# Performance work log

Measured on AMD Instinct MI355X. Metric: run time of the kernel, lower is better.

The kernel has to match this reference:

```python
import jax, jax.numpy as jnp
import numpy as np

# Dropout layers are treated as identity (eval mode) for a deterministic reference.

def _branch(x, Ws):
    # pattern in original: relu -> (dropout) -> linear, repeated; last linear has no trailing relu
    for W in Ws:
        x = jax.nn.relu(x) @ W.T
    return x

def _cross_mul(s, e):
    # z[k,h] = sum_j s[k,h]*e[k,j] = s[k,h] * sum_j e[k,j]
    return s * jnp.sum(e, axis=-1, keepdims=True)

def setup_inputs() -> dict:
    key = jax.random.key(0)
    ks = jax.random.split(key, 12)
    def lin(k, out_d, in_d):
        return jax.random.normal(k, (out_d, in_d), dtype=jnp.float32) * (1.0 / np.sqrt(in_d))
    B = 65536
    return {
        "result": jax.random.normal(ks[0], (B, 4, 768), dtype=jnp.float32),
        "sW1": lin(ks[1], 96, 768), "sW2": lin(ks[2], 48, 96), "sW3": lin(ks[3], 24, 48),
        "sW4": lin(ks[4], 12, 24), "sW5": lin(ks[5], 2, 12),
        "eW1": lin(ks[6], 96, 768), "eW2": lin(ks[7], 48, 96), "eW3": lin(ks[8], 24, 48),
        "eW4": lin(ks[9], 12, 24), "eW5": lin(ks[10], 8, 12),
        "s_seq": jnp.array([0.25, 0.25, 0.25, 0.25], dtype=jnp.float32),
        "s_pair": jnp.array([0.5, 0.5], dtype=jnp.float32),
        "e_seq": jnp.array([0.25, 0.25, 0.25, 0.25], dtype=jnp.float32),
        "e_pair": jnp.array([0.5, 0.5], dtype=jnp.float32),
        "cross_w": jnp.array([0.5, 0.5], dtype=jnp.float32),
    }

def reference(result, sW1, sW2, sW3, sW4, sW5, eW1, eW2, eW3, eW4, eW5,
              s_seq, s_pair, e_seq, e_pair, cross_w):
    sWs = (sW1, sW2, sW3, sW4, sW5)
    eWs = (eW1, eW2, eW3, eW4, eW5)
    # soft attention pools over the 4 "token" slots
    pair_e = result[:, 0, :] * e_pair[0] + result[:, 2, :] * e_pair[1]
    pair_s = result[:, 0, :] * s_pair[0] + result[:, 2, :] * s_pair[1]
    seq_e = jnp.einsum('bsd,s->bd', result, e_seq)
    seq_s = jnp.einsum('bsd,s->bd', result, s_seq)
    pair_e_out = _branch(pair_e, eWs)  # [B, 8]
    pair_s_out = _branch(pair_s, sWs)  # [B, 2]
    seq_e_out = _branch(seq_e, eWs)    # [B, 8]
    seq_s_out = _branch(seq_s, sWs)    # [B, 2]
    pair_cross = _cross_mul(pair_s_out, pair_e_out)
    seq_cross = _cross_mul(seq_s_out, seq_e_out)
    return cross_w[0] * pair_cross + cross_w[1] * seq_cross
```

## Files before the change

kernel.cpp:

```cpp
#include <hip/hip_runtime.h>

typedef _Float16 half8 __attribute__((ext_vector_type(8)));
typedef float floatx4 __attribute__((ext_vector_type(4)));

#define MFMA16(a, b, c) __builtin_amdgcn_mfma_f32_16x16x32_f16((a), (b), (c), 0, 0, 0)

#define OFF_W1 0
#define OFF_W2 147456
#define OFF_W3 156672
#define OFF_W4 160768
#define OFF_W5 161792

typedef __attribute__((address_space(3))) unsigned int lds_uint;
typedef __attribute__((address_space(1))) unsigned int glob_uint;

__device__ __forceinline__ void async_copy16(const void* g, void* l) {
    __builtin_amdgcn_global_load_lds((const glob_uint*)g, (lds_uint*)l, 16, 0, 0);
}

__global__ __launch_bounds__(64) void prep_weights(
    const float* __restrict__ eW1, const float* __restrict__ sW1,
    const float* __restrict__ eW2, const float* __restrict__ sW2,
    const float* __restrict__ eW3, const float* __restrict__ sW3,
    const float* __restrict__ eW4, const float* __restrict__ sW4,
    const float* __restrict__ eW5, const float* __restrict__ sW5,
    _Float16* __restrict__ ws)
{
    int b = blockIdx.x;
    int lane = threadIdx.x;
    const float* src;
    _Float16* dst;
    int N, K, nt, ks;
    if (b < 288) {
        int mat = b / 144, r = b % 144;
        nt = r / 24; ks = r % 24;
        src = mat ? sW1 : eW1; N = 96; K = 768;
        dst = ws + OFF_W1 + (size_t)((mat * 6 + nt) * 24 + ks) * 512;
    } else if (b < 306) {
        int i = b - 288, mat = i / 9, r = i % 9;
        nt = r / 3; ks = r % 3;
        src = mat ? sW2 : eW2; N = 48; K = 96;
        dst = ws + OFF_W2 + (size_t)((mat * 3 + nt) * 3 + ks) * 512;
    } else if (b < 314) {
        int i = b - 306, mat = i / 4, r = i % 4;
        nt = r / 2; ks = r % 2;
        src = mat ? sW3 : eW3; N = 24; K = 48;
        dst = ws + OFF_W3 + (size_t)((mat * 2 + nt) * 2 + ks) * 512;
    } else if (b < 316) {
        int mat = b - 314;
        nt = 0; ks = 0;
        src = mat ? sW4 : eW4; N = 12; K = 24;
        dst = ws + OFF_W4 + (size_t)mat * 512;
    } else {
        int mat = b - 316;
        nt = 0; ks = 0;
        src = mat ? sW5 : eW5; N = mat ? 2 : 8; K = 12;
        dst = ws + OFF_W5 + (size_t)mat * 512;
    }
    int n = nt * 16 + (lane & 15);
    int kb = ks * 32 + (lane >> 4) * 8;
    for (int j = 0; j < 8; ++j) {
        int k = kb + j;
        float v = (n < N && k < K) ? src[n * K + k] : 0.0f;
        dst[lane * 8 + j] = (_Float16)v;
    }
}

__device__ __forceinline__ const float4* rawp(const unsigned char* buf, int s, int t, int k16) {
    return (const float4*)(buf + ((s >> 1) * 1040 + ((s & 1) << 9) + (((t << 3) | k16) << 4)));
}

__device__ __forceinline__ half8 frag_pair(const unsigned char* buf, int s, int q,
                                           float w0, float w1) {
    float4 a0 = *rawp(buf, s, 0, 2 * q);
    float4 a1 = *rawp(buf, s, 0, 2 * q + 1);
    float4 c0 = *rawp(buf, s, 2, 2 * q);
    float4 c1 = *rawp(buf, s, 2, 2 * q + 1);
    half8 h;
    h[0] = (_Float16)fmaxf(w0 * a0.x + w1 * c0.x, 0.f);
    h[1] = (_Float16)fmaxf(w0 * a0.y + w1 * c0.y, 0.f);
    h[2] = (_Float16)fmaxf(w0 * a0.z + w1 * c0.z, 0.f);
    h[3] = (_Float16)fmaxf(w0 * a0.w + w1 * c0.w, 0.f);
    h[4] = (_Float16)fmaxf(w0 * a1.x + w1 * c1.x, 0.f);
    h[5] = (_Float16)fmaxf(w0 * a1.y + w1 * c1.y, 0.f);
    h[6] = (_Float16)fmaxf(w0 * a1.z + w1 * c1.z, 0.f);
    h[7] = (_Float16)fmaxf(w0 * a1.w + w1 * c1.w, 0.f);
    return h;
}

__device__ __forceinline__ half8 frag_seq(const unsigned char* buf, int s, int q,
                                          float w0, float w1, float w2, float w3) {
    float4 a0 = *rawp(buf, s, 0, 2 * q);
    float4 a1 = *rawp(buf, s, 0, 2 * q + 1);
    float4 b0 = *rawp(buf, s, 1, 2 * q);
    float4 b1 = *rawp(buf, s, 1, 2 * q + 1);
    float4 c0 = *rawp(buf, s, 2, 2 * q);
    float4 c1 = *rawp(buf, s, 2, 2 * q + 1);
    float4 d0 = *rawp(buf, s, 3, 2 * q);
    float4 d1 = *rawp(buf, s, 3, 2 * q + 1);
    half8 h;
    h[0] = (_Float16)fmaxf(w0 * a0.x + w1 * b0.x + w2 * c0.x + w3 * d0.x, 0.f);
    h[1] = (_Float16)fmaxf(w0 * a0.y + w1 * b0.y + w2 * c0.y + w3 * d0.y, 0.f);
    h[2] = (_Float16)fmaxf(w0 * a0.z + w1 * b0.z + w2 * c0.z + w3 * d0.z, 0.f);
    h[3] = (_Float16)fmaxf(w0 * a0.w + w1 * b0.w + w2 * c0.w + w3 * d0.w, 0.f);
    h[4] = (_Float16)fmaxf(w0 * a1.x + w1 * b1.x + w2 * c1.x + w3 * d1.x, 0.f);
    h[5] = (_Float16)fmaxf(w0 * a1.y + w1 * b1.y + w2 * c1.y + w3 * d1.y, 0.f);
    h[6] = (_Float16)fmaxf(w0 * a1.z + w1 * b1.z + w2 * c1.z + w3 * d1.z, 0.f);
    h[7] = (_Float16)fmaxf(w0 * a1.w + w1 * b1.w + w2 * c1.w + w3 * d1.w, 0.f);
    return h;
}

__global__ __launch_bounds__(256, 4) void fused_net(
    const float* __restrict__ result,
    const float* __restrict__ e_pair, const float* __restrict__ s_pair,
    const float* __restrict__ e_seq,  const float* __restrict__ s_seq,
    const float* __restrict__ cross_w,
    const _Float16* __restrict__ ws,
    float* __restrict__ out)
{
    __shared__ __align__(16) unsigned char lds_raw[35840];
    float* EoLDS = (float*)(lds_raw + 33280);
    float* SoLDS = (float*)(lds_raw + 33280 + 2048);

    const int tid  = threadIdx.x;
    const int lane = tid & 63;
    const int wave = tid >> 6;
    const int l15  = lane & 15;
    const int q    = lane >> 4;
    const int mat  = wave >> 1;
    const int mh   = wave & 1;
    const int sbase = blockIdx.x * 32;

    float w0, w1, w2 = 0.f, w3 = 0.f;
    if (mh == 0) {
        w0 = mat ? s_pair[0] : e_pair[0];
        w1 = mat ? s_pair[1] : e_pair[1];
    } else {
        w0 = mat ? s_seq[0] : e_seq[0];
        w1 = mat ? s_seq[1] : e_seq[1];
        w2 = mat ? s_seq[2] : e_seq[2];
        w3 = mat ? s_seq[3] : e_seq[3];
    }

    const floatx4 zf4 = {0.f, 0.f, 0.f, 0.f};

    const int dma_so  = lane >> 5;
    const int dma_u   = lane & 31;
    const int dma_t   = dma_u >> 3;
    const int dma_k16 = dma_u & 7;
    const size_t dma_goff = (size_t)(dma_t * 768 + dma_k16 * 4);

    floatx4 acc[2][6];
#pragma unroll
    for (int m = 0; m < 2; ++m)
#pragma unroll
        for (int n = 0; n < 6; ++n) acc[m][n] = zf4;

    const half8* Bw1 = (const half8*)(ws + OFF_W1) + (size_t)mat * (6 * 24 * 64);

    {
        const float* gbase = result + (size_t)sbase * 3072;
#pragma unroll
        for (int i = 0; i < 4; ++i) {
            int blk = wave * 4 + i;
            const float* g = gbase + (size_t)(2 * blk + dma_so) * 3072 + dma_goff;
            async_copy16(g, lds_raw + blk * 1040);
        }
    }
    __syncthreads();

#pragma unroll 2
    for (int c = 0; c < 24; ++c) {
        const unsigned char* cur = lds_raw + (c & 1) * 16640;
        unsigned char* nxt = lds_raw + ((c + 1) & 1) * 16640;
        if (c < 23) {
            const float* gbase = result + (size_t)sbase * 3072 + (c + 1) * 32;
#pragma unroll
            for (int i = 0; i < 4; ++i) {
                int blk = wave * 4 + i;
                const float* g = gbase + (size_t)(2 * blk + dma_so) * 3072 + dma_goff;
                async_copy16(g, nxt + blk * 1040);
            }
        }
        half8 a0f, a1f;
        if (mh == 0) {
            a0f = frag_pair(cur, l15,      q, w0, w1);
            a1f = frag_pair(cur, l15 + 16, q, w0, w1);
        } else {
            a0f = frag_seq(cur, l15,      q, w0, w1, w2, w3);
            a1f = frag_seq(cur, l15 + 16, q, w0, w1, w2, w3);
        }
#pragma unroll
        for (int nt = 0; nt < 6; ++nt) {
            half8 bf = Bw1[(nt * 24 + c) * 64 + lane];
            acc[0][nt] = MFMA16(a0f, bf, acc[0][nt]);
            acc[1][nt] = MFMA16(a1f, bf, acc[1][nt]);
        }
        __syncthreads();
    }

    _Float16* Y = (_Float16*)lds_raw;

#pragma unroll
    for (int m = 0; m < 2; ++m)
#pragma unroll
        for (int nt = 0; nt < 6; ++nt)
#pragma unroll
            for (int r = 0; r < 4; ++r) {
                int row = mat * 64 + mh * 32 + m * 16 + q * 4 + r;
                Y[row * 104 + nt * 16 + l15] = (_Float16)fmaxf(acc[m][nt][r], 0.f);
            }
    __syncthreads();

    floatx4 acc2[2][3];
#pragma unroll
    for (int m = 0; m < 2; ++m)
#pragma unroll
        for (int n = 0; n < 3; ++n) acc2[m][n] = zf4;
    {
        const _Float16* A2 = Y + mat * 64 * 104;
        const half8* Bw2 = (const half8*)(ws + OFF_W2) + (size_t)mat * (3 * 3 * 64);
#pragma unroll
        for (int ks2 = 0; ks2 < 3; ++ks2) {
            half8 a0 = *(const half8*)(A2 + (mh * 32 + l15) * 104 + ks2 * 32 + q * 8);
            half8 a1 = *(const half8*)(A2 + (mh * 32 + 16 + l15) * 104 + ks2 * 32 + q * 8);
#pragma unroll
            for (int nt = 0; nt < 3; ++nt) {
                half8 bf = Bw2[(nt * 3 + ks2) * 64 + lane];
                acc2[0][nt] = MFMA16(a0, bf, acc2[0][nt]);
                acc2[1][nt] = MFMA16(a1, bf, acc2[1][nt]);
            }
        }
    }
    __syncthreads();
#pragma unroll
    for (int m = 0; m < 2; ++m)
#pragma unroll
        for (int nt = 0; nt < 3; ++nt)
#pragma unroll
            for (int r = 0; r < 4; ++r) {
                int row = mat * 64 + mh * 32 + m * 16 + q * 4 + r;
                Y[row * 72 + nt * 16 + l15] = (_Float16)fmaxf(acc2[m][nt][r], 0.f);
            }
    for (int i = tid; i < 2048; i += 256) {
        int row = i >> 4;
        Y[row * 72 + 48 + (i & 15)] = (_Float16)0.f;
    }
    __syncthreads();

    floatx4 acc3[2][2];
#pragma unroll
    for (int m = 0; m < 2; ++m)
#pragma unroll
        for (int n = 0; n < 2; ++n) acc3[m][n] = zf4;
    {
        const _Float16* A3 = Y + mat * 64 * 72;
        const half8* Bw3 = (const half8*)(ws + OFF_W3) + (size_t)mat * (2 * 2 * 64);
#pragma unroll
        for (int ks2 = 0; ks2 < 2; ++ks2) {
            half8 a0 = *(const half8*)(A3 + (mh * 32 + l15) * 72 + ks2 * 32 + q * 8);
            half8 a1 = *(const half8*)(A3 + (mh * 32 + 16 + l15) * 72 + ks2 * 32 + q * 8);
#pragma unroll
            for (int nt = 0; nt < 2; ++nt) {
                half8 bf = Bw3[(nt * 2 + ks2) * 64 + lane];
                acc3[0][nt] = MFMA16(a0, bf, acc3[0][nt]);
                acc3[1][nt] = MFMA16(a1, bf, acc3[1][nt]);
            }
        }
    }
    __syncthreads();
#pragma unroll
    for (int m = 0; m < 2; ++m)
#pragma unroll
        for (int nt = 0; nt < 2; ++nt)
#pragma unroll
            for (int r = 0; r < 4; ++r) {
                int row = mat * 64 + mh * 32 + m * 16 + q * 4 + r;
                Y[row * 40 + nt * 16 + l15] = (_Float16)fmaxf(acc3[m][nt][r], 0.f);
            }
    for (int i = tid; i < 1024; i += 256) {
        int row = i >> 3;
        Y[row * 40 + 24 + (i & 7)] = (_Float16)0.f;
    }
    __syncthreads();

    floatx4 acc4[2];
    {
        const _Float16* A4 = Y + mat * 64 * 40;
        const half8* Bw4 = (const half8*)(ws + OFF_W4) + (size_t)mat * 64;
        half8 a0 = *(const half8*)(A4 + (mh * 32 + l15) * 40 + q * 8);
        half8 a1 = *(const half8*)(A4 + (mh * 32 + 16 + l15) * 40 + q * 8);
        half8 bf = Bw4[lane];
        acc4[0] = MFMA16(a0, bf, zf4);
        acc4[1] = MFMA16(a1, bf, zf4);
    }
    __syncthreads();
#pragma unroll
    for (int m = 0; m < 2; ++m)
#pragma unroll
        for (int r = 0; r < 4; ++r) {
            int row = mat * 64 + mh * 32 + m * 16 + q * 4 + r;
            Y[row * 40 + l15] = (_Float16)fmaxf(acc4[m][r], 0.f);
        }
    for (int i = tid; i < 2560; i += 256) {
        int row = i / 20;
        Y[row * 40 + 12 + (i % 20)] = (_Float16)0.f;
    }
    __syncthreads();

    floatx4 acc5[2];
    {
        const _Float16* A5 = Y + mat * 64 * 40;
        const half8* Bw5 = (const half8*)(ws + OFF_W5) + (size_t)mat * 64;
        half8 a0 = *(const half8*)(A5 + (mh * 32 + l15) * 40 + q * 8);
        half8 a1 = *(const half8*)(A5 + (mh * 32 + 16 + l15) * 40 + q * 8);
        half8 bf = Bw5[lane];
        acc5[0] = MFMA16(a0, bf, zf4);
        acc5[1] = MFMA16(a1, bf, zf4);
    }
    if (mat == 0) {
        if (l15 < 8) {
#pragma unroll
            for (int m = 0; m < 2; ++m)
#pragma unroll
                for (int r = 0; r < 4; ++r) {
                    int row = mh * 32 + m * 16 + q * 4 + r;
                    EoLDS[row * 8 + l15] = acc5[m][r];
                }
        }
    } else {
        if (l15 < 2) {
#pragma unroll
            for (int m = 0; m < 2; ++m)
#pragma unroll
                for (int r = 0; r < 4; ++r) {
                    int row = mh * 32 + m * 16 + q * 4 + r;
                    SoLDS[row * 2 + l15] = acc5[m][r];
                }
        }
    }
    __syncthreads();

    if (tid < 64) {
        int sample = tid >> 1;
        int h = tid & 1;
        float cw0 = cross_w[0], cw1 = cross_w[1];
        float pes = 0.f, ses = 0.f;
#pragma unroll
        for (int j = 0; j < 8; ++j) {
            pes += EoLDS[sample * 8 + j];
            ses += EoLDS[(32 + sample) * 8 + j];
        }
        float v = cw0 * SoLDS[sample * 2 + h] * pes
                + cw1 * SoLDS[(32 + sample) * 2 + h] * ses;
        out[(size_t)(sbase + sample) * 2 + h] = v;
    }
}

extern "C" void kernel_launch(void* const* d_in, const int* in_sizes, int n_in,
                              void* d_out, int out_size, void* d_ws, size_t ws_size,
                              hipStream_t stream) {
    (void)n_in; (void)out_size; (void)ws_size;
    const float* result = (const float*)d_in[0];
    const float* sW1 = (const float*)d_in[1];
    const float* sW2 = (const float*)d_in[2];
    const float* sW3 = (const float*)d_in[3];
    const float* sW4 = (const float*)d_in[4];
    const float* sW5 = (const float*)d_in[5];
    const float* eW1 = (const float*)d_in[6];
    const float* eW2 = (const float*)d_in[7];
    const float* eW3 = (const float*)d_in[8];
    const float* eW4 = (const float*)d_in[9];
    const float* eW5 = (const float*)d_in[10];
    const float* s_seq  = (const float*)d_in[11];
    const float* s_pair = (const float*)d_in[12];
    const float* e_seq  = (const float*)d_in[13];
    const float* e_pair = (const float*)d_in[14];
    const float* cross_w = (const float*)d_in[15];
    _Float16* ws = (_Float16*)d_ws;
    float* out = (float*)d_out;

    int B = in_sizes[0] / 3072;

    prep_weights<<<dim3(318), dim3(64), 0, stream>>>(
        eW1, sW1, eW2, sW2, eW3, sW3, eW4, sW4, eW5, sW5, ws);

    fused_net<<<dim3(B / 32), dim3(256), 0, stream>>>(
        result, e_pair, s_pair, e_seq, s_seq, cross_w, ws, out);
}
```

Before: 1.060 ms.

## Replace LDS double-buffered async staging with direct global loads and wave shuffles

The first-layer input staging no longer uses global_load_lds double buffering into LDS with per-chunk block barriers. Each wave now loads its rows straight from global memory into registers, computes the pooled ReLU values, packs them to fp16, and rearranges them into MFMA fragment layout with cross-lane shuffles. This removes the LDS traffic and the 24 __syncthreads in the K loop and shrinks LDS use. In exchange it loses explicit prefetch overlap, adds shuffle work, and all four waves now load the input independently (pair and seq waves reread the same data), raising global/L2 traffic. The occupancy hint drops from 4 to 3 blocks per SIMD.

```diff
diff --git a/kernel.cpp b/kernel.cpp
--- a/kernel.cpp
+++ b/kernel.cpp
@@ -10,13 +10,6 @@
 #define OFF_W3 156672
 #define OFF_W4 160768
 #define OFF_W5 161792
-
-typedef __attribute__((address_space(3))) unsigned int lds_uint;
-typedef __attribute__((address_space(1))) unsigned int glob_uint;
-
-__device__ __forceinline__ void async_copy16(const void* g, void* l) {
-    __builtin_amdgcn_global_load_lds((const glob_uint*)g, (lds_uint*)l, 16, 0, 0);
-}
 
 __global__ __launch_bounds__(64) void prep_weights(
     const float* __restrict__ eW1, const float* __restrict__ sW1,
@@ -66,51 +59,14 @@
     }
 }
 
-__device__ __forceinline__ const float4* rawp(const unsigned char* buf, int s, int t, int k16) {
-    return (const float4*)(buf + ((s >> 1) * 1040 + ((s & 1) << 9) + (((t << 3) | k16) << 4)));
+__device__ __forceinline__ unsigned int packh(float a, float b) {
+    union { _Float16 h[2]; unsigned int u; } x;
+    x.h[0] = (_Float16)a;
+    x.h[1] = (_Float16)b;
+    return x.u;
 }
 
-__device__ __forceinline__ half8 frag_pair(const unsigned char* buf, int s, int q,
-                                           float w0, float w1) {
-    float4 a0 = *rawp(buf, s, 0, 2 * q);
-    float4 a1 = *rawp(buf, s, 0, 2 * q + 1);
-    float4 c0 = *rawp(buf, s, 2, 2 * q);
-    float4 c1 = *rawp(buf, s, 2, 2 * q + 1);
-    half8 h;
-    h[0] = (_Float16)fmaxf(w0 * a0.x + w1 * c0.x, 0.f);
-    h[1] = (_Float16)fmaxf(w0 * a0.y + w1 * c0.y, 0.f);
-    h[2] = (_Float16)fmaxf(w0 * a0.z + w1 * c0.z, 0.f);
-    h[3] = (_Float16)fmaxf(w0 * a0.w + w1 * c0.w, 0.f);
-    h[4] = (_Float16)fmaxf(w0 * a1.x + w1 * c1.x, 0.f);
-    h[5] = (_Float16)fmaxf(w0 * a1.y + w1 * c1.y, 0.f);
-    h[6] = (_Float16)fmaxf(w0 * a1.z + w1 * c1.z, 0.f);
-    h[7] = (_Float16)fmaxf(w0 * a1.w + w1 * c1.w, 0.f);
-    return h;
-}
-
-__device__ __forceinline__ half8 frag_seq(const unsigned char* buf, int s, int q,
-                                          float w0, float w1, float w2, float w3) {
-    float4 a0 = *rawp(buf, s, 0, 2 * q);
-    float4 a1 = *rawp(buf, s, 0, 2 * q + 1);
-    float4 b0 = *rawp(buf, s, 1, 2 * q);
-    float4 b1 = *rawp(buf, s, 1, 2 * q + 1);
-    float4 c0 = *rawp(buf, s, 2, 2 * q);
-    float4 c1 = *rawp(buf, s, 2, 2 * q + 1);
-    float4 d0 = *rawp(buf, s, 3, 2 * q);
-    float4 d1 = *rawp(buf, s, 3, 2 * q + 1);
-    half8 h;
-    h[0] = (_Float16)fmaxf(w0 * a0.x + w1 * b0.x + w2 * c0.x + w3 * d0.x, 0.f);
-    h[1] = (_Float16)fmaxf(w0 * a0.y + w1 * b0.y + w2 * c0.y + w3 * d0.y, 0.f);
-    h[2] = (_Float16)fmaxf(w0 * a0.z + w1 * b0.z + w2 * c0.z + w3 * d0.z, 0.f);
-    h[3] = (_Float16)fmaxf(w0 * a0.w + w1 * b0.w + w2 * c0.w + w3 * d0.w, 0.f);
-    h[4] = (_Float16)fmaxf(w0 * a1.x + w1 * b1.x + w2 * c1.x + w3 * d1.x, 0.f);
-    h[5] = (_Float16)fmaxf(w0 * a1.y + w1 * b1.y + w2 * c1.y + w3 * d1.y, 0.f);
-    h[6] = (_Float16)fmaxf(w0 * a1.z + w1 * b1.z + w2 * c1.z + w3 * d1.z, 0.f);
-    h[7] = (_Float16)fmaxf(w0 * a1.w + w1 * b1.w + w2 * c1.w + w3 * d1.w, 0.f);
-    return h;
-}
-
-__global__ __launch_bounds__(256, 4) void fused_net(
+__global__ __launch_bounds__(256, 3) void fused_net(
     const float* __restrict__ result,
     const float* __restrict__ e_pair, const float* __restrict__ s_pair,
     const float* __restrict__ e_seq,  const float* __restrict__ s_seq,
@@ -118,9 +74,9 @@
     const _Float16* __restrict__ ws,
     float* __restrict__ out)
 {
-    __shared__ __align__(16) unsigned char lds_raw[35840];
-    float* EoLDS = (float*)(lds_raw + 33280);
-    float* SoLDS = (float*)(lds_raw + 33280 + 2048);
+    __shared__ __align__(16) unsigned char lds_raw[29184];
+    float* EoLDS = (float*)(lds_raw + 26624);
+    float* SoLDS = (float*)(lds_raw + 26624 + 2048);
 
     const int tid  = threadIdx.x;
     const int lane = tid & 63;
@@ -144,12 +100,6 @@
 
     const floatx4 zf4 = {0.f, 0.f, 0.f, 0.f};
 
-    const int dma_so  = lane >> 5;
-    const int dma_u   = lane & 31;
-    const int dma_t   = dma_u >> 3;
-    const int dma_k16 = dma_u & 7;
-    const size_t dma_goff = (size_t)(dma_t * 768 + dma_k16 * 4);
-
     floatx4 acc[2][6];
 #pragma unroll
     for (int m = 0; m < 2; ++m)
@@ -158,45 +108,66 @@
 
     const half8* Bw1 = (const half8*)(ws + OFF_W1) + (size_t)mat * (6 * 24 * 64);
 
-    {
-        const float* gbase = result + (size_t)sbase * 3072;
-#pragma unroll
-        for (int i = 0; i < 4; ++i) {
-            int blk = wave * 4 + i;
-            const float* g = gbase + (size_t)(2 * blk + dma_so) * 3072 + dma_goff;
-            async_copy16(g, lds_raw + blk * 1040);
-        }
-    }
-    __syncthreads();
-
-#pragma unroll 2
-    for (int c = 0; c < 24; ++c) {
-        const unsigned char* cur = lds_raw + (c & 1) * 16640;
-        unsigned char* nxt = lds_raw + ((c + 1) & 1) * 16640;
-        if (c < 23) {
-            const float* gbase = result + (size_t)sbase * 3072 + (c + 1) * 32;
-#pragma unroll
-            for (int i = 0; i < 4; ++i) {
-                int blk = wave * 4 + i;
-                const float* g = gbase + (size_t)(2 * blk + dma_so) * 3072 + dma_goff;
-                async_copy16(g, nxt + blk * 1040);
-            }
-        }
-        half8 a0f, a1f;
-        if (mh == 0) {
-            a0f = frag_pair(cur, l15,      q, w0, w1);
-            a1f = frag_pair(cur, l15 + 16, q, w0, w1);
-        } else {
-            a0f = frag_seq(cur, l15,      q, w0, w1, w2, w3);
-            a1f = frag_seq(cur, l15 + 16, q, w0, w1, w2, w3);
+    const int ls  = lane >> 3;
+    const int lj4 = lane & 7;
+    const float* rb0 = result + (size_t)(sbase + ls) * 3072 + lj4 * 4;
+
+    const int src0 = ((l15 & 7) << 3) | (q << 1);
+    const int src1 = src0 + 1;
+    const bool hiHalf = (l15 >> 3) != 0;
+
+    for (int kc = 0; kc < 24; ++kc) {
+        half8 afrag[2];
+        const float* rk = rb0 + kc * 32;
+#pragma unroll
+        for (int gg = 0; gg < 2; ++gg) {
+            const float* g0 = rk + (size_t)gg * 16 * 3072;
+            const float* g1 = g0 + 8 * 3072;
+            floatx4 pA, pB;
+            if (mh == 0) {
+                floatx4 a0 = *(const floatx4*)(g0);
+                floatx4 c0 = *(const floatx4*)(g0 + 2 * 768);
+                floatx4 a1 = *(const floatx4*)(g1);
+                floatx4 c1 = *(const floatx4*)(g1 + 2 * 768);
+                pA = w0 * a0 + w1 * c0;
+                pB = w0 * a1 + w1 * c1;
+            } else {
+                floatx4 a0 = *(const floatx4*)(g0);
+                floatx4 b0 = *(const floatx4*)(g0 + 768);
+                floatx4 c0 = *(const floatx4*)(g0 + 2 * 768);
+                floatx4 d0 = *(const floatx4*)(g0 + 3 * 768);
+                floatx4 a1 = *(const floatx4*)(g1);
+                floatx4 b1 = *(const floatx4*)(g1 + 768);
+                floatx4 c1 = *(const floatx4*)(g1 + 2 * 768);
+                floatx4 d1 = *(const floatx4*)(g1 + 3 * 768);
+                pA = w0 * a0 + w1 * b0 + w2 * c0 + w3 * d0;
+                pB = w0 * a1 + w1 * b1 + w2 * c1 + w3 * d1;
+            }
+            unsigned int uL0 = packh(fmaxf(pA[0], 0.f), fmaxf(pA[1], 0.f));
+            unsigned int uL1 = packh(fmaxf(pA[2], 0.f), fmaxf(pA[3], 0.f));
+            unsigned int uH0 = packh(fmaxf(pB[0], 0.f), fmaxf(pB[1], 0.f));
+            unsigned int uH1 = packh(fmaxf(pB[2], 0.f), fmaxf(pB[3], 0.f));
+            unsigned int w0L = (unsigned int)__shfl((int)uL0, src0);
+            unsigned int w0H = (unsigned int)__shfl((int)uH0, src0);
+            unsigned int w1L = (unsigned int)__shfl((int)uL1, src0);
+            unsigned int w1H = (unsigned int)__shfl((int)uH1, src0);
+            unsigned int w2L = (unsigned int)__shfl((int)uL0, src1);
+            unsigned int w2H = (unsigned int)__shfl((int)uH0, src1);
+            unsigned int w3L = (unsigned int)__shfl((int)uL1, src1);
+            unsigned int w3H = (unsigned int)__shfl((int)uH1, src1);
+            union { unsigned int u[4]; half8 h; } f;
+            f.u[0] = hiHalf ? w0H : w0L;
+            f.u[1] = hiHalf ? w1H : w1L;
+            f.u[2] = hiHalf ? w2H : w2L;
+            f.u[3] = hiHalf ? w3H : w3L;
+            afrag[gg] = f.h;
         }
 #pragma unroll
         for (int nt = 0; nt < 6; ++nt) {
-            half8 bf = Bw1[(nt * 24 + c) * 64 + lane];
-            acc[0][nt] = MFMA16(a0f, bf, acc[0][nt]);
-            acc[1][nt] = MFMA16(a1f, bf, acc[1][nt]);
-        }
-        __syncthreads();
+            half8 bf = Bw1[(nt * 24 + kc) * 64 + lane];
+            acc[0][nt] = MFMA16(afrag[0], bf, acc[0][nt]);
+            acc[1][nt] = MFMA16(afrag[1], bf, acc[1][nt]);
+        }
     }
 
     _Float16* Y = (_Float16*)lds_raw;
```

Result: slower. 1.122 ms (+5.8%).
